# Kernel tuning notes

Hardware: AMD Instinct MI355X
Metric: run time of the kernel (lower is better)

Reference implementation:

```python
import jax, jax.numpy as jnp
import numpy as np
from jax import lax

B, QL, VL, D, H, K = 8, 512, 2048, 1024, 8, 10
DH = D // H  # per-head dim = 128


def setup_inputs() -> dict:
    key = jax.random.key(0)
    ks = jax.random.split(key, 12)
    s = 0.02
    return {
        "Q": jax.random.normal(ks[0], (B, QL, D), jnp.float32),
        "V": jax.random.normal(ks[1], (B, VL, D), jnp.float32),
        "last_align": jax.random.uniform(ks[2], (B, QL), jnp.float32),
        "conv_w": jax.random.normal(ks[3], (K, 1, 3), jnp.float32) * s,
        "conv_b": jnp.zeros((K,), jnp.float32),
        "Wq": jax.random.normal(ks[4], (D, D), jnp.float32) * s,
        "bq": jnp.zeros((D,), jnp.float32),
        "Wv": jax.random.normal(ks[5], (D, D), jnp.float32) * s,
        "bv": jnp.zeros((D,), jnp.float32),
        "Wu": jax.random.normal(ks[6], (D, K), jnp.float32) * s,
        "bu": jnp.zeros((D,), jnp.float32),
        "bias": jax.random.uniform(ks[7], (D,), jnp.float32, -0.1, 0.1),
        "fc_w": jax.random.normal(ks[8], (D, 2 * D), jnp.float32) * s,
        "fc_b": jnp.zeros((D,), jnp.float32),
    }


def reference(Q, V, last_align, conv_w, conv_b, Wq, bq, Wv, bv, Wu, bu, bias, fc_w, fc_b):
    b, qlen, d_model = Q.shape
    vlen = V.shape[1]
    # location feature: conv1d over last_align -> (B, K, qlen) -> (B, qlen, K)
    u = lax.conv_general_dilated(last_align[:, None, :], conv_w, (1,), [(1, 1)],
                                 dimension_numbers=("NCH", "OIH", "NCH"))
    U = jnp.transpose(u + conv_b[None, :, None], (0, 2, 1))  # (B, qlen, K)
    # fused projections + bias adds
    q_s = Q @ Wq.T + bq + U @ Wu.T + bu + bias  # (B, qlen, D)
    v_s = V @ Wv.T + bv                          # (B, vlen, D)
    q_s = q_s.reshape(b, qlen, H, DH)
    v_s = v_s.reshape(b, vlen, H, DH)
    score = jnp.einsum("bqhd,bvhd->bhqv", q_s, v_s) / np.sqrt(DH).astype(jnp.float32)
    # sigmoid smoothing normalization (not softmax)
    score = jax.nn.sigmoid(score)
    align = score / jnp.sum(score, axis=-1, keepdims=True)  # (B, H, qlen, vlen)
    context = jnp.einsum("bhqv,bvhd->bqhd", align, v_s).reshape(b, qlen, d_model)
    combined = jnp.concatenate([context, Q], axis=-1)  # (B, qlen, 2D)
    output = jnp.tanh(combined @ fc_w.T + fc_b)        # (B, qlen, D)
    # torch returns align flattened head-major: (H*B, qlen, vlen)
    align_t = jnp.transpose(align, (1, 0, 2, 3)).reshape(H * b, qlen, vlen)
    return output, align_t
```

## Files before the change

kernel.cpp:

```cpp
#include <hip/hip_runtime.h>

typedef __attribute__((ext_vector_type(8))) short short8;
typedef __attribute__((ext_vector_type(4))) short short4v;
typedef __attribute__((ext_vector_type(4))) float f32x4;

static __device__ __forceinline__ short f2bf(float x) {
    unsigned u = __builtin_bit_cast(unsigned, x);
    unsigned r = (u + 0x7fffu + ((u >> 16) & 1u)) >> 16;
    return (short)r;
}

static __device__ __forceinline__ void gld16(const short* g, short* l) {
    __builtin_amdgcn_global_load_lds((const __attribute__((address_space(1))) void*)g,
                                     (__attribute__((address_space(3))) void*)l, 16, 0, 0);
}

#define QL 512
#define VL 2048
#define DM 1024
#define NH 8
#define DH 128
#define NB 8
#define KQ 1088

#define KSIG (-0.12751542401539644f)

__global__ void prep_k(const float* __restrict__ Q, const float* __restrict__ V,
                       const float* __restrict__ la, const float* __restrict__ cw,
                       const float* __restrict__ cb,
                       const float* __restrict__ Wq, const float* __restrict__ bq,
                       const float* __restrict__ Wv, const float* __restrict__ Wu,
                       const float* __restrict__ bu, const float* __restrict__ bias,
                       const float* __restrict__ fcw,
                       float* __restrict__ cbias, short* __restrict__ Aq,
                       short* __restrict__ comb, short* __restrict__ Vb,
                       short* __restrict__ Bq, short* __restrict__ Bv,
                       short* __restrict__ Bfc) {
    const int blk = blockIdx.x, tid = threadIdx.x;
    if (blk < 4) {
        int i = blk * 256 + tid;
        if (i < DM) cbias[i] = bq[i] + bu[i] + bias[i];
    } else if (blk < 20) {
        int m = (blk - 4) * 256 + tid;
        if (m >= NB * QL) return;
        int b = m >> 9, t = m & 511;
        const float* l = la + b * QL;
        float lm = (t > 0)      ? l[t - 1] : 0.f;
        float l0 = l[t];
        float lp = (t < QL - 1) ? l[t + 1] : 0.f;
        short* row = Aq + (size_t)m * KQ + 1024;
#pragma unroll
        for (int k = 0; k < 10; ++k)
            row[k] = f2bf(cb[k] + lm * cw[k * 3 + 0] + l0 * cw[k * 3 + 1] + lp * cw[k * 3 + 2]);
        for (int k = 10; k < 64; ++k) row[k] = 0;
    } else if (blk < 2068) {
        int id = (blk - 20) * 256 + tid;
        int m = id >> 7, kc = (id & 127) * 8;
        const float* p = Q + (size_t)m * DM + kc;
        float4 f0 = *(const float4*)p;
        float4 f1 = *(const float4*)(p + 4);
        short8 v;
        v[0]=f2bf(f0.x); v[1]=f2bf(f0.y); v[2]=f2bf(f0.z); v[3]=f2bf(f0.w);
        v[4]=f2bf(f1.x); v[5]=f2bf(f1.y); v[6]=f2bf(f1.z); v[7]=f2bf(f1.w);
        *(short8*)(Aq + (size_t)m * KQ + kc) = v;
        *(short8*)(comb + (size_t)m * (2 * DM) + DM + kc) = v;
    } else if (blk < 10260) {
        int id = (blk - 2068) * 256 + tid;
        const float* p = V + (size_t)id * 8;
        float4 f0 = *(const float4*)p;
        float4 f1 = *(const float4*)(p + 4);
        short8 v;
        v[0]=f2bf(f0.x); v[1]=f2bf(f0.y); v[2]=f2bf(f0.z); v[3]=f2bf(f0.w);
        v[4]=f2bf(f1.x); v[5]=f2bf(f1.y); v[6]=f2bf(f1.z); v[7]=f2bf(f1.w);
        *(short8*)(Vb + (size_t)id * 8) = v;
    } else {
        int id = (blk - 10260) * 256 + tid;
        const int nq = DM * KQ;
        const int nv = DM * DM;
        const int nf = DM * 2 * DM;
        if (id < nq) {
            int n = id / KQ, k = id % KQ;
            float v = (k < 1024) ? Wq[(size_t)n * 1024 + k]
                                 : ((k < 1034) ? Wu[n * 10 + (k - 1024)] : 0.f);
            Bq[id] = f2bf(v);
        } else if (id < nq + nv) {
            int j = id - nq;
            Bv[j] = f2bf(Wv[j]);
        } else if (id < nq + nv + nf) {
            int j = id - nq - nv;
            Bfc[j] = f2bf(fcw[j]);
        }
    }
}

template <int MODE>
static __device__ __forceinline__ void gemm_body(
    short* As, short* Bs,
    const short* __restrict__ A, const short* __restrict__ B,
    const float* __restrict__ bias, void* __restrict__ out0,
    short* __restrict__ outT, int K, int out_ld, int bm, int bn) {
    const int tid = threadIdx.x;
    const int lane = tid & 63, wave = tid >> 6;
    const int g = lane >> 4, c = lane & 15;
    const int wr = wave >> 1, wc = wave & 1;

    const int srow = lane >> 3, scol = (lane & 7) * 8;
    const short* ag = A + (size_t)(bm * 128 + wave * 32 + srow) * K + scol;
    const short* bg = B + (size_t)(bn * 128 + wave * 32 + srow) * K + scol;

    f32x4 acc[4][4] = {};
    for (int k0 = 0; k0 < K; k0 += 64) {
#pragma unroll
        for (int ch = 0; ch < 4; ++ch) {
            gld16(ag + (size_t)(ch * 8) * K + k0, As + (wave * 32 + ch * 8) * 64);
            gld16(bg + (size_t)(ch * 8) * K + k0, Bs + (wave * 32 + ch * 8) * 64);
        }
        __syncthreads();
#pragma unroll
        for (int ks = 0; ks < 2; ++ks) {
            short8 af[4], bfr[4];
#pragma unroll
            for (int mi = 0; mi < 4; ++mi) af[mi] = *(const short8*)(As + (wr * 64 + mi * 16 + c) * 64 + ks * 32 + g * 8);
#pragma unroll
            for (int ni = 0; ni < 4; ++ni) bfr[ni] = *(const short8*)(Bs + (wc * 64 + ni * 16 + c) * 64 + ks * 32 + g * 8);
#pragma unroll
            for (int mi = 0; mi < 4; ++mi)
#pragma unroll
                for (int ni = 0; ni < 4; ++ni)
                    acc[mi][ni] = __builtin_amdgcn_mfma_f32_16x16x32_bf16(af[mi], bfr[ni], acc[mi][ni], 0, 0, 0);
        }
        __syncthreads();
    }

    const int m0 = bm * 128 + wr * 64, n0 = bn * 128 + wc * 64;
#pragma unroll
    for (int ni = 0; ni < 4; ++ni) {
        int n = n0 + ni * 16 + c;
        float bn_ = bias[n];
#pragma unroll
        for (int mi = 0; mi < 4; ++mi) {
            int mb = m0 + mi * 16 + 4 * g;
            f32x4 v = acc[mi][ni];
            if constexpr (MODE == 2) {
                float* o = (float*)out0;
#pragma unroll
                for (int r = 0; r < 4; ++r)
                    o[(size_t)(mb + r) * out_ld + n] = tanhf(v[r] + bn_);
            } else {
                short* o = (short*)out0;
                short4v pk;
#pragma unroll
                for (int r = 0; r < 4; ++r) {
                    pk[r] = f2bf(v[r] + bn_);
                    o[(size_t)(mb + r) * out_ld + n] = pk[r];
                }
                if constexpr (MODE == 0) {
                    int h = n >> 7, hd = n & 127;
                    int bb = mb >> 11, vv = mb & 2047;
                    *(short4v*)(outT + ((size_t)((bb * NH + h) * DH + hd)) * VL + vv) = pk;
                }
            }
        }
    }
}

__global__ __launch_bounds__(256) void gemmvq_k(
    const short* __restrict__ Vb, const short* __restrict__ Bvw,
    const float* __restrict__ bv, short* __restrict__ vsb, short* __restrict__ vsT,
    const short* __restrict__ Aq, const short* __restrict__ Bq,
    const float* __restrict__ cbias, short* __restrict__ qsb) {
    __shared__ short As[128 * 64];
    __shared__ short Bs[128 * 64];
    const int blk = blockIdx.x;
    if (blk < 1024) {
        const int x = blk & 7, j = blk >> 3;
        gemm_body<0>(As, Bs, Vb, Bvw, bv, vsb, vsT, 1024, 1024, x * 16 + (j >> 3), j & 7);
    } else {
        const int b2 = blk - 1024;
        const int x = b2 & 7, j = b2 >> 3;
        gemm_body<1>(As, Bs, Aq, Bq, cbias, qsb, nullptr, KQ, 1024, x * 4 + (j >> 3), j & 7);
    }
}

__global__ __launch_bounds__(256) void gemmfc_k(
    const short* __restrict__ comb, const short* __restrict__ Bfc,
    const float* __restrict__ fcb, float* __restrict__ out) {
    __shared__ short As[128 * 64];
    __shared__ short Bs[128 * 64];
    const int x = blockIdx.x & 7, j = blockIdx.x >> 3;
    gemm_body<2>(As, Bs, comb, Bfc, fcb, out, nullptr, 2048, 1024, x * 4 + (j >> 3), j & 7);
}

__global__ __launch_bounds__(256) void rowsum_k(
    const short* __restrict__ qs, const short* __restrict__ vs,
    float* __restrict__ rsum_part) {
    __shared__ short As[128 * 64];
    __shared__ short Bs[128 * 64];
    const int blk = blockIdx.x;
    const int xr = blk & 7, t = blk >> 3;
    const int bn = t & 15;
    const int bm = (t >> 4) & 3;
    const int bh = ((t >> 6) << 3) | xr;
    const int h = bh & 7, b = bh >> 3;

    const int tid = threadIdx.x;
    const int lane = tid & 63, wave = tid >> 6;
    const int g = lane >> 4, c = lane & 15;
    const int wr = wave >> 1, wc = wave & 1;

    const int srow = lane >> 3, scol = (lane & 7) * 8;
    const short* ag = qs + (size_t)(b * QL + bm * 128 + wave * 32 + srow) * DM + h * DH + scol;
    const short* bg = vs + (size_t)(b * VL + bn * 128 + wave * 32 + srow) * DM + h * DH + scol;

    f32x4 acc[4][4] = {};
    for (int k0 = 0; k0 < DH; k0 += 64) {
#pragma unroll
        for (int ch = 0; ch < 4; ++ch) {
            gld16(ag + (size_t)(ch * 8) * DM + k0, As + (wave * 32 + ch * 8) * 64);
            gld16(bg + (size_t)(ch * 8) * DM + k0, Bs + (wave * 32 + ch * 8) * 64);
        }
        __syncthreads();
#pragma unroll
        for (int ks = 0; ks < 2; ++ks) {
            short8 af[4], bfr[4];
#pragma unroll
            for (int mi = 0; mi < 4; ++mi) af[mi] = *(const short8*)(As + (wr * 64 + mi * 16 + c) * 64 + ks * 32 + g * 8);
#pragma unroll
            for (int ni = 0; ni < 4; ++ni) bfr[ni] = *(const short8*)(Bs + (wc * 64 + ni * 16 + c) * 64 + ks * 32 + g * 8);
#pragma unroll
            for (int mi = 0; mi < 4; ++mi)
#pragma unroll
                for (int ni = 0; ni < 4; ++ni)
                    acc[mi][ni] = __builtin_amdgcn_mfma_f32_16x16x32_bf16(af[mi], bfr[ni], acc[mi][ni], 0, 0, 0);
        }
        __syncthreads();
    }

    float psum[4][4];
#pragma unroll
    for (int mi = 0; mi < 4; ++mi)
#pragma unroll
        for (int r = 0; r < 4; ++r) psum[mi][r] = 0.f;

    const int m0 = bm * 128 + wr * 64;
#pragma unroll
    for (int ni = 0; ni < 4; ++ni) {
#pragma unroll
        for (int mi = 0; mi < 4; ++mi) {
            f32x4 v = acc[mi][ni];
#pragma unroll
            for (int r = 0; r < 4; ++r)
                psum[mi][r] += __builtin_amdgcn_rcpf(1.f + __builtin_amdgcn_exp2f(v[r] * KSIG));
        }
    }
#pragma unroll
    for (int off = 1; off < 16; off <<= 1)
#pragma unroll
        for (int mi = 0; mi < 4; ++mi)
#pragma unroll
            for (int r = 0; r < 4; ++r) psum[mi][r] += __shfl_xor(psum[mi][r], off);
    if (c == 0) {
#pragma unroll
        for (int mi = 0; mi < 4; ++mi)
#pragma unroll
            for (int r = 0; r < 4; ++r) {
                int q = m0 + mi * 16 + 4 * g + r;
                rsum_part[(size_t)(bh * QL + q) * 32 + bn * 2 + wc] = psum[mi][r];
            }
    }
}

__global__ __launch_bounds__(256, 3) void fat2_k(
    const short* __restrict__ qs, const short* __restrict__ vs,
    const short* __restrict__ vsT, const float* __restrict__ rsum_part,
    float* __restrict__ align_out, short* __restrict__ ctxp) {
    __shared__ short Vs[64][136];
    __shared__ short Vt[128][72];
    __shared__ short Pl[4][16][72];
    __shared__ float rsl[64];

    const int blk = blockIdx.x;
    const int xr = blk & 7, t = blk >> 3;
    const int vh = t & 1;
    const int qt = (t >> 1) & 7;
    const int bh = ((t >> 4) << 3) | xr;
    const int h = bh & 7, b = bh >> 3;
    const int q0 = qt * 64;
    const int vbeg = vh * 1024;

    const int tid = threadIdx.x, wave = tid >> 6, lane = tid & 63;
    const int g = lane >> 4, c = lane & 15;

    if (tid < 64) {
        const float* p = rsum_part + (size_t)(bh * QL + q0 + tid) * 32;
        float s = 0.f;
#pragma unroll
        for (int jj = 0; jj < 32; ++jj) s += p[jj];
        rsl[tid] = __builtin_amdgcn_rcpf(s);
    }
    __syncthreads();

    float invr[4];
#pragma unroll
    for (int r = 0; r < 4; ++r) invr[r] = rsl[wave * 16 + 4 * g + r];

    short8 qa[4];
    const short* qb = qs + ((size_t)(b * QL + q0 + wave * 16 + c)) * DM + h * DH + g * 8;
#pragma unroll
    for (int ks = 0; ks < 4; ++ks) qa[ks] = *(const short8*)(qb + ks * 32);

    const int vsrow = tid >> 2, vscq = (tid & 3) * 32;
    const short* vsg = vs + ((size_t)(b * VL + vsrow)) * DM + h * DH + vscq;
    const int vtrow = tid >> 1, vtcq = (tid & 1) * 32;
    const short* vtg = vsT + ((size_t)(bh * DH + vtrow)) * VL + vtcq;

    float* ao = align_out + ((size_t)((h * NB + b) * QL + q0 + wave * 16)) * VL;

    short8 pv_s[4], pv_t[4];
#pragma unroll
    for (int i = 0; i < 4; ++i) pv_s[i] = *(const short8*)(vsg + (size_t)vbeg * DM + i * 8);
#pragma unroll
    for (int i = 0; i < 4; ++i) pv_t[i] = *(const short8*)(vtg + vbeg + i * 8);

    f32x4 ctx[8] = {};
    for (int tc = 0; tc < 16; ++tc) {
        const int v0 = vbeg + tc * 64;
#pragma unroll
        for (int i = 0; i < 4; ++i) *(short8*)&Vs[vsrow][vscq + i * 8] = pv_s[i];
#pragma unroll
        for (int i = 0; i < 4; ++i) *(short8*)&Vt[vtrow][vtcq + i * 8] = pv_t[i];
        __syncthreads();
        if (tc + 1 < 16) {
            const int v1 = v0 + 64;
#pragma unroll
            for (int i = 0; i < 4; ++i) pv_s[i] = *(const short8*)(vsg + (size_t)v1 * DM + i * 8);
#pragma unroll
            for (int i = 0; i < 4; ++i) pv_t[i] = *(const short8*)(vtg + v1 + i * 8);
        }

#pragma unroll
        for (int ni = 0; ni < 4; ++ni) {
            f32x4 s = {0.f, 0.f, 0.f, 0.f};
#pragma unroll
            for (int ks = 0; ks < 4; ++ks)
                s = __builtin_amdgcn_mfma_f32_16x16x32_bf16(qa[ks], *(const short8*)&Vs[ni * 16 + c][ks * 32 + g * 8], s, 0, 0, 0);
#pragma unroll
            for (int r = 0; r < 4; ++r) {
                float pn = __builtin_amdgcn_rcpf(1.f + __builtin_amdgcn_exp2f(s[r] * KSIG)) * invr[r];
                __builtin_nontemporal_store(pn, &ao[(size_t)(4 * g + r) * VL + v0 + ni * 16 + c]);
                Pl[wave][4 * g + r][ni * 16 + c] = f2bf(pn);
            }
        }
        short8 pa0 = *(const short8*)&Pl[wave][c][g * 8];
        short8 pa1 = *(const short8*)&Pl[wave][c][32 + g * 8];
#pragma unroll
        for (int df = 0; df < 8; ++df) {
            ctx[df] = __builtin_amdgcn_mfma_f32_16x16x32_bf16(pa0, *(const short8*)&Vt[df * 16 + c][g * 8], ctx[df], 0, 0, 0);
            ctx[df] = __builtin_amdgcn_mfma_f32_16x16x32_bf16(pa1, *(const short8*)&Vt[df * 16 + c][32 + g * 8], ctx[df], 0, 0, 0);
        }
        __syncthreads();
    }

    short* cp = ctxp + ((size_t)((bh * 8 + qt) * 2 + vh)) * (64 * 128);
#pragma unroll
    for (int df = 0; df < 8; ++df)
#pragma unroll
        for (int r = 0; r < 4; ++r)
            cp[(size_t)(wave * 16 + 4 * g + r) * 128 + df * 16 + c] = f2bf(ctx[df][r]);
}

__global__ void ctxred_k(const short* __restrict__ ctxp, short* __restrict__ comb) {
    int id = blockIdx.x * 256 + threadIdx.x;
    int d0 = (id & 15) * 8;
    int r  = (id >> 4) & 63;
    int qt = (id >> 10) & 7;
    int bh = id >> 13;
    int h = bh & 7, b = bh >> 3;
    const short* p0 = ctxp + ((size_t)((bh * 8 + qt) * 2)) * 8192 + r * 128 + d0;
    const short* p1 = p0 + 8192;
    short8 a = *(const short8*)p0;
    short8 bb = *(const short8*)p1;
    short8 o;
#pragma unroll
    for (int jj = 0; jj < 8; ++jj) {
        float fa = __builtin_bit_cast(float, ((unsigned)(unsigned short)a[jj]) << 16);
        float fb = __builtin_bit_cast(float, ((unsigned)(unsigned short)bb[jj]) << 16);
        o[jj] = f2bf(fa + fb);
    }
    *(short8*)(comb + ((size_t)(b * QL + qt * 64 + r)) * (2 * DM) + h * DH + d0) = o;
}

extern "C" void kernel_launch(void* const* d_in, const int* in_sizes, int n_in,
                              void* d_out, int out_size, void* d_ws, size_t ws_size,
                              hipStream_t stream) {
    (void)in_sizes; (void)n_in; (void)out_size; (void)ws_size;
    const float* Q    = (const float*)d_in[0];
    const float* V    = (const float*)d_in[1];
    const float* la   = (const float*)d_in[2];
    const float* cw   = (const float*)d_in[3];
    const float* cb   = (const float*)d_in[4];
    const float* Wq   = (const float*)d_in[5];
    const float* bq   = (const float*)d_in[6];
    const float* Wv   = (const float*)d_in[7];
    const float* bv   = (const float*)d_in[8];
    const float* Wu   = (const float*)d_in[9];
    const float* bu   = (const float*)d_in[10];
    const float* bias = (const float*)d_in[11];
    const float* fcw  = (const float*)d_in[12];
    const float* fcb  = (const float*)d_in[13];

    float* out = (float*)d_out;
    float* align_out = out + (size_t)NB * QL * DM;

    char* w = (char*)d_ws;
    short* Vb   = (short*)w; w += (size_t)16384 * 1024 * 2;
    short* Aq   = (short*)w; w += (size_t)4096 * KQ * 2;
    short* comb = (short*)w; w += (size_t)4096 * 2048 * 2;
    short* Bq   = (short*)w; w += (size_t)1024 * KQ * 2;
    short* Bvw  = (short*)w; w += (size_t)1024 * 1024 * 2;
    short* Bfc  = (short*)w; w += (size_t)1024 * 2048 * 2;
    short* vsb  = (short*)w; w += (size_t)16384 * 1024 * 2;
    short* vsT  = (short*)w; w += (size_t)16384 * 1024 * 2;
    short* qsb  = (short*)w; w += (size_t)4096 * 1024 * 2;
    float* rsum_part = (float*)w; w += (size_t)32768 * 32 * 4;
    short* ctxp = (short*)w; w += (size_t)1024 * 64 * 128 * 2;
    float* cbias = (float*)w; w += 1024 * 4;

    prep_k<<<26900, 256, 0, stream>>>(Q, V, la, cw, cb, Wq, bq, Wv, Wu, bu, bias, fcw,
                                      cbias, Aq, comb, Vb, Bq, Bvw, Bfc);
    gemmvq_k<<<1280, 256, 0, stream>>>(Vb, Bvw, bv, vsb, vsT, Aq, Bq, cbias, qsb);
    rowsum_k<<<4096, 256, 0, stream>>>(qsb, vsb, rsum_part);
    fat2_k<<<1024, 256, 0, stream>>>(qsb, vsb, vsT, rsum_part, align_out, ctxp);
    ctxred_k<<<2048, 256, 0, stream>>>(ctxp, comb);
    gemmfc_k<<<256, 256, 0, stream>>>(comb, Bfc, fcb, out);
}
```

Measured before the change: 293.6 us.

## Store sigmoid scores in bf16 during row-sum pass and reuse them for align and context

The row-sum kernel now writes the unnormalized sigmoid scores as bf16 into a workspace buffer. A new attention kernel reads those scores back, scales them into the fp32 align output and feeds them into the P·V MFMA, instead of recomputing Q·Vᵀ and the sigmoid. Normalization of the context moves to the final write. This removes the second QK matmul and sigmoid evaluation. In exchange it adds a large write and read of the score matrix, and the align output is now derived from bf16-rounded scores. If the workspace is too small, the work runs in four chunks that reuse the Vb buffer.

```diff
diff --git a/kernel.cpp b/kernel.cpp
--- a/kernel.cpp
+++ b/kernel.cpp
@@ -8,6 +8,9 @@
     unsigned u = __builtin_bit_cast(unsigned, x);
     unsigned r = (u + 0x7fffu + ((u >> 16) & 1u)) >> 16;
     return (short)r;
+}
+static __device__ __forceinline__ float bf2f(short s) {
+    return __builtin_bit_cast(float, ((unsigned)(unsigned short)s) << 16);
 }
 
 static __device__ __forceinline__ void gld16(const short* g, short* l) {
@@ -193,14 +196,15 @@
 
 __global__ __launch_bounds__(256) void rowsum_k(
     const short* __restrict__ qs, const short* __restrict__ vs,
-    float* __restrict__ rsum_part) {
+    float* __restrict__ rsum_part, short* __restrict__ pbuf, int bh_lo) {
     __shared__ short As[128 * 64];
     __shared__ short Bs[128 * 64];
     const int blk = blockIdx.x;
     const int xr = blk & 7, t = blk >> 3;
     const int bn = t & 15;
     const int bm = (t >> 4) & 3;
-    const int bh = ((t >> 6) << 3) | xr;
+    const int bh_rel = ((t >> 6) << 3) | xr;
+    const int bh = bh_lo + bh_rel;
     const int h = bh & 7, b = bh >> 3;
 
     const int tid = threadIdx.x;
@@ -243,14 +247,19 @@
         for (int r = 0; r < 4; ++r) psum[mi][r] = 0.f;
 
     const int m0 = bm * 128 + wr * 64;
+    const int n0 = bn * 128 + wc * 64;
+    short* pb = pbuf + (size_t)(bh_rel * QL) * VL;
 #pragma unroll
     for (int ni = 0; ni < 4; ++ni) {
 #pragma unroll
         for (int mi = 0; mi < 4; ++mi) {
             f32x4 v = acc[mi][ni];
 #pragma unroll
-            for (int r = 0; r < 4; ++r)
-                psum[mi][r] += __builtin_amdgcn_rcpf(1.f + __builtin_amdgcn_exp2f(v[r] * KSIG));
+            for (int r = 0; r < 4; ++r) {
+                float p = __builtin_amdgcn_rcpf(1.f + __builtin_amdgcn_exp2f(v[r] * KSIG));
+                psum[mi][r] += p;
+                pb[(size_t)(m0 + mi * 16 + 4 * g + r) * VL + n0 + ni * 16 + c] = f2bf(p);
+            }
         }
     }
 #pragma unroll
@@ -270,20 +279,20 @@
     }
 }
 
-__global__ __launch_bounds__(256, 3) void fat2_k(
-    const short* __restrict__ qs, const short* __restrict__ vs,
-    const short* __restrict__ vsT, const float* __restrict__ rsum_part,
-    float* __restrict__ align_out, short* __restrict__ ctxp) {
-    __shared__ short Vs[64][136];
+__global__ __launch_bounds__(256) void fat3_k(
+    const short* __restrict__ pbuf, const short* __restrict__ vsT,
+    const float* __restrict__ rsum_part, float* __restrict__ align_out,
+    short* __restrict__ ctxp, int bh_lo) {
+    __shared__ short Pl[64][72];
     __shared__ short Vt[128][72];
-    __shared__ short Pl[4][16][72];
     __shared__ float rsl[64];
 
     const int blk = blockIdx.x;
     const int xr = blk & 7, t = blk >> 3;
     const int vh = t & 1;
     const int qt = (t >> 1) & 7;
-    const int bh = ((t >> 4) << 3) | xr;
+    const int bh_rel = ((t >> 4) << 3) | xr;
+    const int bh = bh_lo + bh_rel;
     const int h = bh & 7, b = bh >> 3;
     const int q0 = qt * 64;
     const int vbeg = vh * 1024;
@@ -300,59 +309,59 @@
     }
     __syncthreads();
 
+    const int prow = tid >> 2, pcq = (tid & 3) * 16;
+    const float invt = rsl[prow];
+    const short* pg = pbuf + ((size_t)(bh_rel * QL + q0 + prow)) * VL + pcq;
+    float* ao = align_out + ((size_t)((h * NB + b) * QL + q0 + prow)) * VL + pcq;
+
     float invr[4];
 #pragma unroll
     for (int r = 0; r < 4; ++r) invr[r] = rsl[wave * 16 + 4 * g + r];
 
-    short8 qa[4];
-    const short* qb = qs + ((size_t)(b * QL + q0 + wave * 16 + c)) * DM + h * DH + g * 8;
-#pragma unroll
-    for (int ks = 0; ks < 4; ++ks) qa[ks] = *(const short8*)(qb + ks * 32);
-
-    const int vsrow = tid >> 2, vscq = (tid & 3) * 32;
-    const short* vsg = vs + ((size_t)(b * VL + vsrow)) * DM + h * DH + vscq;
     const int vtrow = tid >> 1, vtcq = (tid & 1) * 32;
     const short* vtg = vsT + ((size_t)(bh * DH + vtrow)) * VL + vtcq;
 
-    float* ao = align_out + ((size_t)((h * NB + b) * QL + q0 + wave * 16)) * VL;
-
-    short8 pv_s[4], pv_t[4];
-#pragma unroll
-    for (int i = 0; i < 4; ++i) pv_s[i] = *(const short8*)(vsg + (size_t)vbeg * DM + i * 8);
-#pragma unroll
-    for (int i = 0; i < 4; ++i) pv_t[i] = *(const short8*)(vtg + vbeg + i * 8);
+    short8 pp[2], pt[4];
+    pp[0] = *(const short8*)(pg + vbeg);
+    pp[1] = *(const short8*)(pg + vbeg + 8);
+#pragma unroll
+    for (int i = 0; i < 4; ++i) pt[i] = *(const short8*)(vtg + vbeg + i * 8);
 
     f32x4 ctx[8] = {};
     for (int tc = 0; tc < 16; ++tc) {
         const int v0 = vbeg + tc * 64;
-#pragma unroll
-        for (int i = 0; i < 4; ++i) *(short8*)&Vs[vsrow][vscq + i * 8] = pv_s[i];
-#pragma unroll
-        for (int i = 0; i < 4; ++i) *(short8*)&Vt[vtrow][vtcq + i * 8] = pv_t[i];
-        __syncthreads();
+        *(short8*)&Pl[prow][pcq] = pp[0];
+        *(short8*)&Pl[prow][pcq + 8] = pp[1];
+#pragma unroll
+        for (int i = 0; i < 4; ++i) *(short8*)&Vt[vtrow][vtcq + i * 8] = pt[i];
+        __syncthreads();
+
+        {
+            f32x4 o0, o1, o2, o3;
+            o0[0] = bf2f(pp[0][0]) * invt; o0[1] = bf2f(pp[0][1]) * invt;
+            o0[2] = bf2f(pp[0][2]) * invt; o0[3] = bf2f(pp[0][3]) * invt;
+            o1[0] = bf2f(pp[0][4]) * invt; o1[1] = bf2f(pp[0][5]) * invt;
+            o1[2] = bf2f(pp[0][6]) * invt; o1[3] = bf2f(pp[0][7]) * invt;
+            o2[0] = bf2f(pp[1][0]) * invt; o2[1] = bf2f(pp[1][1]) * invt;
+            o2[2] = bf2f(pp[1][2]) * invt; o2[3] = bf2f(pp[1][3]) * invt;
+            o3[0] = bf2f(pp[1][4]) * invt; o3[1] = bf2f(pp[1][5]) * invt;
+            o3[2] = bf2f(pp[1][6]) * invt; o3[3] = bf2f(pp[1][7]) * invt;
+            float* a = ao + v0;
+            __builtin_nontemporal_store(o0, (f32x4*)(a));
+            __builtin_nontemporal_store(o1, (f32x4*)(a + 4));
+            __builtin_nontemporal_store(o2, (f32x4*)(a + 8));
+            __builtin_nontemporal_store(o3, (f32x4*)(a + 12));
+        }
         if (tc + 1 < 16) {
             const int v1 = v0 + 64;
-#pragma unroll
-            for (int i = 0; i < 4; ++i) pv_s[i] = *(const short8*)(vsg + (size_t)v1 * DM + i * 8);
-#pragma unroll
-            for (int i = 0; i < 4; ++i) pv_t[i] = *(const short8*)(vtg + v1 + i * 8);
-        }
-
-#pragma unroll
-        for (int ni = 0; ni < 4; ++ni) {
-            f32x4 s = {0.f, 0.f, 0.f, 0.f};
-#pragma unroll
-            for (int ks = 0; ks < 4; ++ks)
-                s = __builtin_amdgcn_mfma_f32_16x16x32_bf16(qa[ks], *(const short8*)&Vs[ni * 16 + c][ks * 32 + g * 8], s, 0, 0, 0);
-#pragma unroll
-            for (int r = 0; r < 4; ++r) {
-                float pn = __builtin_amdgcn_rcpf(1.f + __builtin_amdgcn_exp2f(s[r] * KSIG)) * invr[r];
-                __builtin_nontemporal_store(pn, &ao[(size_t)(4 * g + r) * VL + v0 + ni * 16 + c]);
-                Pl[wave][4 * g + r][ni * 16 + c] = f2bf(pn);
-            }
-        }
-        short8 pa0 = *(const short8*)&Pl[wave][c][g * 8];
-        short8 pa1 = *(const short8*)&Pl[wave][c][32 + g * 8];
+            pp[0] = *(const short8*)(pg + v1);
+            pp[1] = *(const short8*)(pg + v1 + 8);
+#pragma unroll
+            for (int i = 0; i < 4; ++i) pt[i] = *(const short8*)(vtg + v1 + i * 8);
+        }
+
+        short8 pa0 = *(const short8*)&Pl[wave * 16 + c][g * 8];
+        short8 pa1 = *(const short8*)&Pl[wave * 16 + c][32 + g * 8];
 #pragma unroll
         for (int df = 0; df < 8; ++df) {
             ctx[df] = __builtin_amdgcn_mfma_f32_16x16x32_bf16(pa0, *(const short8*)&Vt[df * 16 + c][g * 8], ctx[df], 0, 0, 0);
@@ -366,7 +375,7 @@
     for (int df = 0; df < 8; ++df)
 #pragma unroll
         for (int r = 0; r < 4; ++r)
-            cp[(size_t)(wave * 16 + 4 * g + r) * 128 + df * 16 + c] = f2bf(ctx[df][r]);
+            cp[(size_t)(wave * 16 + 4 * g + r) * 128 + df * 16 + c] = f2bf(ctx[df][r] * invr[r]);
 }
 
 __global__ void ctxred_k(const short* __restrict__ ctxp, short* __restrict__ comb) {
@@ -382,18 +391,15 @@
     short8 bb = *(const short8*)p1;
     short8 o;
 #pragma unroll
-    for (int jj = 0; jj < 8; ++jj) {
-        float fa = __builtin_bit_cast(float, ((unsigned)(unsigned short)a[jj]) << 16);
-        float fb = __builtin_bit_cast(float, ((unsigned)(unsigned short)bb[jj]) << 16);
-        o[jj] = f2bf(fa + fb);
-    }
+    for (int jj = 0; jj < 8; ++jj)
+        o[jj] = f2bf(bf2f(a[jj]) + bf2f(bb[jj]));
     *(short8*)(comb + ((size_t)(b * QL + qt * 64 + r)) * (2 * DM) + h * DH + d0) = o;
 }
 
 extern "C" void kernel_launch(void* const* d_in, const int* in_sizes, int n_in,
                               void* d_out, int out_size, void* d_ws, size_t ws_size,
                               hipStream_t stream) {
-    (void)in_sizes; (void)n_in; (void)out_size; (void)ws_size;
+    (void)in_sizes; (void)n_in; (void)out_size;
     const float* Q    = (const float*)d_in[0];
     const float* V    = (const float*)d_in[1];
     const float* la   = (const float*)d_in[2];
@@ -413,6 +419,7 @@
     float* align_out = out + (size_t)NB * QL * DM;
 
     char* w = (char*)d_ws;
+    char* w0 = w;
     short* Vb   = (short*)w; w += (size_t)16384 * 1024 * 2;
     short* Aq   = (short*)w; w += (size_t)4096 * KQ * 2;
     short* comb = (short*)w; w += (size_t)4096 * 2048 * 2;
@@ -425,12 +432,24 @@
     float* rsum_part = (float*)w; w += (size_t)32768 * 32 * 4;
     short* ctxp = (short*)w; w += (size_t)1024 * 64 * 128 * 2;
     float* cbias = (float*)w; w += 1024 * 4;
+    short* pbuf_flat = (short*)w;
+    size_t need_flat = (size_t)(w - w0) + (size_t)64 * QL * VL * 2;
+    bool flat = ws_size >= need_flat;
 
     prep_k<<<26900, 256, 0, stream>>>(Q, V, la, cw, cb, Wq, bq, Wv, Wu, bu, bias, fcw,
                                       cbias, Aq, comb, Vb, Bq, Bvw, Bfc);
     gemmvq_k<<<1280, 256, 0, stream>>>(Vb, Bvw, bv, vsb, vsT, Aq, Bq, cbias, qsb);
-    rowsum_k<<<4096, 256, 0, stream>>>(qsb, vsb, rsum_part);
-    fat2_k<<<1024, 256, 0, stream>>>(qsb, vsb, vsT, rsum_part, align_out, ctxp);
+
+    if (flat) {
+        rowsum_k<<<4096, 256, 0, stream>>>(qsb, vsb, rsum_part, pbuf_flat, 0);
+        fat3_k<<<1024, 256, 0, stream>>>(pbuf_flat, vsT, rsum_part, align_out, ctxp, 0);
+    } else {
+        short* pbuf4 = Vb;
+        for (int p = 0; p < 4; ++p) {
+            rowsum_k<<<1024, 256, 0, stream>>>(qsb, vsb, rsum_part, pbuf4, p * 16);
+            fat3_k<<<256, 256, 0, stream>>>(pbuf4, vsT, rsum_part, align_out, ctxp, p * 16);
+        }
+    }
     ctxred_k<<<2048, 256, 0, stream>>>(ctxp, comb);
     gemmfc_k<<<256, 256, 0, stream>>>(comb, Bfc, fcb, out);
 }
```

Result: slower. 501.8 us (+70.9%).
